# Optimization experiments

Hardware: AMD Instinct MI355X
Metric: run time of the kernel (lower is better)

The kernel has to match this reference:

```python
import jax, jax.numpy as jnp
import numpy as np

NUM_FREQ = 4
MAX_FREQ_LOG2 = 10.0
# standard NeRF frequency bands: 2^linspace(0, max_freq_log2, num_freq)
FREQ_BANDS = 2.0 ** np.linspace(0.0, MAX_FREQ_LOG2, NUM_FREQ).astype(np.float32)


def positional_encoding(x):
    # x: [N, 3] -> [N, 3*(1 + 2*num_freq)] = [N, 27]
    xf = x[..., None, :] * jnp.asarray(FREQ_BANDS, dtype=x.dtype)[:, None]  # [N, F, 3]
    enc = jnp.concatenate([jnp.sin(xf), jnp.cos(xf)], axis=-1)  # [N, F, 6]
    return jnp.concatenate([x, enc.reshape(x.shape[0], -1)], axis=-1)


def setup_inputs() -> dict:
    key = jax.random.key(0)
    k1, k2, k3 = jax.random.split(key, 3)
    N = 2097152
    x = jax.random.normal(k1, (N, 3), dtype=jnp.float32)
    in_dim, hidden = 27, 32
    # torch Linear default init scale ~ 1/sqrt(fan_in)
    W1 = jax.random.normal(k2, (in_dim, hidden), dtype=jnp.float32) / np.sqrt(in_dim)
    b1 = jnp.zeros((hidden,), dtype=jnp.float32)
    W2 = jax.random.normal(k3, (hidden, 1), dtype=jnp.float32) / np.sqrt(hidden)
    b2 = jnp.zeros((1,), dtype=jnp.float32)
    return {"x": x, "W1": W1, "b1": b1, "W2": W2, "b2": b2}


def reference(x, W1, b1, W2, b2):
    t = positional_encoding(x)                    # [N, 27]
    h = jax.nn.relu(t @ W1 + b1)                  # [N, 32]
    out = jax.nn.relu(h @ W2 + b2)                # [N, 1]
    return out
```

## Files before the change

### kernel.cpp

```cpp
#include <hip/hip_runtime.h>


#define NPTS  2097152
#define BLOCK 256
#define TILES 4
#define NBLK  (NPTS / (BLOCK * TILES))
#define TABN  4096

typedef __bf16 bf16x8 __attribute__((ext_vector_type(8)));
typedef float  f32x8  __attribute__((ext_vector_type(8)));
typedef float  f32x4  __attribute__((ext_vector_type(4)));

__global__ __launch_bounds__(BLOCK, 8) void nerf_tab(
    const float* __restrict__ x,
    const float* __restrict__ W1,
    const float* __restrict__ b1,
    const float* __restrict__ W2,
    const float* __restrict__ b2,
    float* __restrict__ out)
{
    __shared__ float stab[TABN];

    const int tid  = threadIdx.x;
    const int wave = tid >> 6;
    const int lane = tid & 63;
    const int g    = lane >> 4;
    const int c    = lane & 15;

    #pragma unroll
    for (int i = 0; i < TABN / BLOCK; ++i) {
        const int idx = tid + i * BLOCK;
        stab[idx] = __builtin_amdgcn_sinf((float)idx * (1.0f / TABN));
    }

    const float INV2PI = 0.15915494309189535f;
    float Fg = 1.0f;
    Fg = (g == 1) ? 10.079368f : Fg;
    Fg = (g == 2) ? 101.59367f : Fg;
    Fg = (g == 3) ? 1024.0f    : Fg;
    const float FgN = Fg * INV2PI * (float)TABN;

    bf16x8 afrag[2];
    #pragma unroll
    for (int mt = 0; mt < 2; ++mt) {
        const int j = mt * 16 + c;
        f32x8 af;
        #pragma unroll
        for (int i = 0; i < 3; ++i) af[i] = W1[(3 + 6 * g + i) * 32 + j];
        #pragma unroll
        for (int i = 3; i < 6; ++i) af[i] = W1[(6 + 6 * g + (i - 3)) * 32 + j];
        af[6] = (g < 3) ? W1[g * 32 + j] : b1[j];
        af[7] = 0.0f;
        afrag[mt] = __builtin_convertvector(af, bf16x8);
    }
    bf16x8 a2;
    {
        f32x8 a2f;
        #pragma unroll
        for (int i = 0; i < 4; ++i) {
            a2f[i]     = W2[4 * g + i];
            a2f[4 + i] = W2[16 + 4 * g + i];
        }
        a2 = __builtin_convertvector(a2f, bf16x8);
    }
    const float bias2 = b2[0];
    const f32x4 Z = {0.f, 0.f, 0.f, 0.f};

    __syncthreads();

    const int tbase = blockIdx.x * (4 * TILES) + wave * TILES;

    #pragma unroll
    for (int t = 0; t < TILES; ++t) {
        const float3* xb3 = (const float3*)(x + (size_t)(tbase + t) * 192);
        float3 P[4];
        #pragma unroll
        for (int nt = 0; nt < 4; ++nt) P[nt] = xb3[16 * nt + c];

        float p[4];
        #pragma unroll
        for (int nt = 0; nt < 4; ++nt) {
            const float x0 = P[nt].x, x1 = P[nt].y, x2 = P[nt].z;

            const int i0 = (int)(x0 * FgN);
            const int i1 = (int)(x1 * FgN);
            const int i2 = (int)(x2 * FgN);

            float extra = x0;
            extra = (g == 1) ? x1 : extra;
            extra = (g == 2) ? x2 : extra;
            extra = (g == 3) ? 1.0f : extra;

            f32x8 bff;
            bff[0] = stab[i0 & (TABN - 1)];
            bff[1] = stab[i1 & (TABN - 1)];
            bff[2] = stab[i2 & (TABN - 1)];
            bff[3] = stab[(i0 + TABN / 4) & (TABN - 1)];
            bff[4] = stab[(i1 + TABN / 4) & (TABN - 1)];
            bff[5] = stab[(i2 + TABN / 4) & (TABN - 1)];
            bff[6] = extra;
            bff[7] = 0.0f;
            const bf16x8 bf = __builtin_convertvector(bff, bf16x8);

            const f32x4 acc0 =
                __builtin_amdgcn_mfma_f32_16x16x32_bf16(afrag[0], bf, Z, 0, 0, 0);
            const f32x4 acc1 =
                __builtin_amdgcn_mfma_f32_16x16x32_bf16(afrag[1], bf, Z, 0, 0, 0);

            f32x8 hf;
            #pragma unroll
            for (int r = 0; r < 4; ++r) {
                hf[r]     = fmaxf(acc0[r], 0.0f);
                hf[4 + r] = fmaxf(acc1[r], 0.0f);
            }
            const bf16x8 h8 = __builtin_convertvector(hf, bf16x8);
            const f32x4 o =
                __builtin_amdgcn_mfma_f32_16x16x32_bf16(a2, h8, Z, 0, 0, 0);
            p[nt] = o[0];
        }

        float v = p[0];
        v = (g == 1) ? p[1] : v;
        v = (g == 2) ? p[2] : v;
        v = (g == 3) ? p[3] : v;
        out[(size_t)(tbase + t) * 64 + lane] = fmaxf(v + bias2, 0.0f);
    }
}

extern "C" void kernel_launch(void* const* d_in, const int* in_sizes, int n_in,
                              void* d_out, int out_size, void* d_ws, size_t ws_size,
                              hipStream_t stream) {
    const float* x  = (const float*)d_in[0];
    const float* W1 = (const float*)d_in[1];
    const float* b1 = (const float*)d_in[2];
    const float* W2 = (const float*)d_in[3];
    const float* b2 = (const float*)d_in[4];
    float* out = (float*)d_out;

    nerf_tab<<<NBLK, BLOCK, 0, stream>>>(x, W1, b1, W2, b2, out);
}
```

Baseline: 21.53 us.

## Pack sin/cos bf16 pairs in LDS table and stage weights in shared memory

The lookup table now stores a packed bf16 sin/cos pair per entry, so each coordinate needs one LDS read instead of two, and the bf16 conversion happens once when the table is built. The W1 fragment is reordered to interleave sin and cos to match the packed layout. Weights, b1 and W2 are loaded cooperatively into shared memory with float4 loads instead of scattered global loads per lane. Launch bounds drop from 8 to 4 waves-per-EU hint, and shared memory per block grows, which may reduce occupancy.

After: 19.98 us. -7.2%, faster.

```diff
diff --git a/kernel.cpp b/kernel.cpp
--- a/kernel.cpp
+++ b/kernel.cpp
@@ -8,10 +8,14 @@
 #define TABN  4096
 
 typedef __bf16 bf16x8 __attribute__((ext_vector_type(8)));
+typedef __bf16 bf16x2 __attribute__((ext_vector_type(2)));
 typedef float  f32x8  __attribute__((ext_vector_type(8)));
 typedef float  f32x4  __attribute__((ext_vector_type(4)));
+typedef float  f32x2  __attribute__((ext_vector_type(2)));
+typedef unsigned int u32;
+typedef u32 u32x4 __attribute__((ext_vector_type(4)));
 
-__global__ __launch_bounds__(BLOCK, 8) void nerf_tab(
+__global__ __launch_bounds__(BLOCK, 4) void nerf_ptab(
     const float* __restrict__ x,
     const float* __restrict__ W1,
     const float* __restrict__ b1,
@@ -19,7 +23,8 @@
     const float* __restrict__ b2,
     float* __restrict__ out)
 {
-    __shared__ float stab[TABN];
+    __shared__ u32 stab[TABN];
+    __shared__ __align__(16) float ws[928];
 
     const int tid  = threadIdx.x;
     const int wave = tid >> 6;
@@ -27,10 +32,22 @@
     const int g    = lane >> 4;
     const int c    = lane & 15;
 
+    if (tid < 232) {
+        float4 v;
+        if (tid < 216)      v = ((const float4*)W1)[tid];
+        else if (tid < 224) v = ((const float4*)b1)[tid - 216];
+        else                v = ((const float4*)W2)[tid - 224];
+        ((float4*)ws)[tid] = v;
+    }
+
     #pragma unroll
     for (int i = 0; i < TABN / BLOCK; ++i) {
         const int idx = tid + i * BLOCK;
-        stab[idx] = __builtin_amdgcn_sinf((float)idx * (1.0f / TABN));
+        const float a = (float)idx * (1.0f / TABN);
+        f32x2 sc;
+        sc[0] = __builtin_amdgcn_sinf(a);
+        sc[1] = __builtin_amdgcn_cosf(a);
+        stab[idx] = __builtin_bit_cast(u32, __builtin_convertvector(sc, bf16x2));
     }
 
     const float INV2PI = 0.15915494309189535f;
@@ -40,16 +57,22 @@
     Fg = (g == 3) ? 1024.0f    : Fg;
     const float FgN = Fg * INV2PI * (float)TABN;
 
+    const float bias2 = b2[0];
+    const f32x4 Z = {0.f, 0.f, 0.f, 0.f};
+
+    __syncthreads();
+
     bf16x8 afrag[2];
     #pragma unroll
     for (int mt = 0; mt < 2; ++mt) {
         const int j = mt * 16 + c;
         f32x8 af;
         #pragma unroll
-        for (int i = 0; i < 3; ++i) af[i] = W1[(3 + 6 * g + i) * 32 + j];
-        #pragma unroll
-        for (int i = 3; i < 6; ++i) af[i] = W1[(6 + 6 * g + (i - 3)) * 32 + j];
-        af[6] = (g < 3) ? W1[g * 32 + j] : b1[j];
+        for (int m = 0; m < 3; ++m) {
+            af[2 * m]     = ws[(3 + 6 * g + m) * 32 + j];
+            af[2 * m + 1] = ws[(6 + 6 * g + m) * 32 + j];
+        }
+        af[6] = (g < 3) ? ws[g * 32 + j] : ws[864 + j];
         af[7] = 0.0f;
         afrag[mt] = __builtin_convertvector(af, bf16x8);
     }
@@ -58,15 +81,11 @@
         f32x8 a2f;
         #pragma unroll
         for (int i = 0; i < 4; ++i) {
-            a2f[i]     = W2[4 * g + i];
-            a2f[4 + i] = W2[16 + 4 * g + i];
+            a2f[i]     = ws[896 + 4 * g + i];
+            a2f[4 + i] = ws[896 + 16 + 4 * g + i];
         }
         a2 = __builtin_convertvector(a2f, bf16x8);
     }
-    const float bias2 = b2[0];
-    const f32x4 Z = {0.f, 0.f, 0.f, 0.f};
-
-    __syncthreads();
 
     const int tbase = blockIdx.x * (4 * TILES) + wave * TILES;
 
@@ -85,22 +104,18 @@
             const int i0 = (int)(x0 * FgN);
             const int i1 = (int)(x1 * FgN);
             const int i2 = (int)(x2 * FgN);
-
             float extra = x0;
             extra = (g == 1) ? x1 : extra;
             extra = (g == 2) ? x2 : extra;
             extra = (g == 3) ? 1.0f : extra;
 
-            f32x8 bff;
-            bff[0] = stab[i0 & (TABN - 1)];
-            bff[1] = stab[i1 & (TABN - 1)];
-            bff[2] = stab[i2 & (TABN - 1)];
-            bff[3] = stab[(i0 + TABN / 4) & (TABN - 1)];
-            bff[4] = stab[(i1 + TABN / 4) & (TABN - 1)];
-            bff[5] = stab[(i2 + TABN / 4) & (TABN - 1)];
-            bff[6] = extra;
-            bff[7] = 0.0f;
-            const bf16x8 bf = __builtin_convertvector(bff, bf16x8);
+            u32x4 uu;
+            uu[0] = stab[i0 & (TABN - 1)];
+            uu[1] = stab[i1 & (TABN - 1)];
+            uu[2] = stab[i2 & (TABN - 1)];
+            f32x2 ex = {extra, 0.0f};
+            uu[3] = __builtin_bit_cast(u32, __builtin_convertvector(ex, bf16x2));
+            const bf16x8 bf = __builtin_bit_cast(bf16x8, uu);
 
             const f32x4 acc0 =
                 __builtin_amdgcn_mfma_f32_16x16x32_bf16(afrag[0], bf, Z, 0, 0, 0);
@@ -137,5 +152,5 @@
     const float* b2 = (const float*)d_in[4];
     float* out = (float*)d_out;
 
-    nerf_tab<<<NBLK, BLOCK, 0, stream>>>(x, W1, b1, W2, b2, out);
+    nerf_ptab<<<NBLK, BLOCK, 0, stream>>>(x, W1, b1, W2, b2, out);
 }
```
